# Optimization experiments

Measured on AMD Instinct MI355X. Metric: run time of the kernel, lower is better.

Reference implementation:

```python
import jax, jax.numpy as jnp
import numpy as np

H = 1024      # hidden_dim
NH = 8        # num_heads
DH = H // NH  # head dim = 128
IN = 512      # in_state_dim
CD = 256      # cond_dim
OUT = 512     # out_motion_dim
FH = 128      # FiLM hidden (hard-coded in _CondFiLM)
CLIP = 16.0   # input_clip
B, T = 2048, 32


def _ln(x, g, b, eps=1e-5):
    m = jnp.mean(x, axis=-1, keepdims=True)
    v = jnp.var(x, axis=-1, keepdims=True)
    return (x - m) * jax.lax.rsqrt(v + eps) * g + b


def setup_inputs() -> dict:
    key = jax.random.key(0)
    ks = jax.random.split(key, 16)
    w = lambda k, s: jax.random.normal(k, s, dtype=jnp.float32) * 0.02
    D = IN + CD
    return {
        'state': jax.random.normal(ks[0], (B, T, IN), dtype=jnp.float32),
        'cond': jax.random.normal(ks[1], (B, T, CD), dtype=jnp.float32),
        # shared_encoder: [Linear -> LayerNorm -> ReLU] x 2
        'ew1': w(ks[2], (D, H)), 'eb1': jnp.zeros((H,)), 'eg1': jnp.ones((H,)), 'ebt1': jnp.zeros((H,)),
        'ew2': w(ks[3], (H, H)), 'eb2': jnp.zeros((H,)), 'eg2': jnp.ones((H,)), 'ebt2': jnp.zeros((H,)),
        # residual_proj (input_dim != hidden_dim -> Linear)
        'rw': w(ks[4], (D, H)), 'rb': jnp.zeros((H,)),
        # FiLM conditioner
        'fw1': w(ks[5], (CD, FH)), 'fb1': jnp.zeros((FH,)),
        'fw2': w(ks[6], (FH, 2 * H)), 'fb2': jnp.zeros((2 * H,)),
        # query LayerNorm
        'lnq_g': jnp.ones((H,)), 'lnq_b': jnp.zeros((H,)),
        # attention projections (bias=False)
        'wq': w(ks[7], (H, H)), 'wk': w(ks[8], (H, H)), 'wv': w(ks[9], (H, H)), 'wo': w(ks[10], (H, H)),
        # coupling norm
        'cn_g': jnp.ones((H,)), 'cn_b': jnp.zeros((H,)),
        # motion head: Linear -> ReLU -> Linear
        'hw1': w(ks[11], (H, H)), 'hb1': jnp.zeros((H,)),
        'hw2': w(ks[12], (H, OUT)), 'hb2': jnp.zeros((OUT,)),
    }


def reference(state, cond, ew1, eb1, eg1, ebt1, ew2, eb2, eg2, ebt2, rw, rb,
              fw1, fb1, fw2, fb2, lnq_g, lnq_b, wq, wk, wv, wo, cn_g, cn_b,
              hw1, hb1, hw2, hb2):
    # input concat + guard clamp
    x = jnp.clip(jnp.concatenate([state, cond], axis=-1), -CLIP, CLIP)  # [B,T,D]
    # shared encoder
    h = jax.nn.relu(_ln(x @ ew1 + eb1, eg1, ebt1))
    h = jax.nn.relu(_ln(h @ ew2 + eb2, eg2, ebt2))                       # [B,T,H]
    res = x @ rw + rb                                                    # [B,T,H]
    # FiLM gain/bias from cond (exact-erf gelu to match torch F.gelu)
    fh = jax.nn.gelu(cond @ fw1 + fb1, approximate=False)
    g, b = jnp.split(fh @ fw2 + fb2, 2, axis=-1)
    g = 1.0 + 0.5 * jnp.tanh(g)
    b = 0.5 * jnp.tanh(b)
    # FiLM-gated query path
    qin = _ln(h, lnq_g, lnq_b) * g + b
    Bq, Tq, _ = h.shape
    q = (qin @ wq).reshape(Bq, Tq, NH, DH)
    k = (h @ wk).reshape(Bq, Tq, NH, DH)
    v = (h @ wv).reshape(Bq, Tq, NH, DH)
    scores = jnp.einsum('bqhd,bkhd->bhqk', q, k) / np.float32(np.sqrt(DH))
    attn = jax.nn.softmax(scores, axis=-1)
    o = jnp.einsum('bhqk,bkhd->bqhd', attn, v).reshape(Bq, Tq, H) @ wo
    # residual couple + norm
    h2 = _ln(h + o + res, cn_g, cn_b)
    # motion head
    m = jax.nn.relu(h2 @ hw1 + hb1)
    return m @ hw2 + hb2  # [B,T,out_motion_dim]
```

## Files before the change

### kernel.cpp

```cpp
#include <hip/hip_runtime.h>
#include <hip/hip_bf16.h>

typedef unsigned short u16;
typedef short bf16x8 __attribute__((ext_vector_type(8)));
typedef u16 u16x8 __attribute__((ext_vector_type(8)));
typedef float f32x4 __attribute__((ext_vector_type(4)));
typedef float f32x16 __attribute__((ext_vector_type(16)));

#define DEV __device__ __forceinline__

DEV u16 f2bf(float f) {
  union { float f; unsigned u; } a; a.f = f;
  unsigned r = a.u + 0x7FFFu + ((a.u >> 16) & 1u);
  return (u16)(r >> 16);
}
DEV float bf2f(u16 u) {
  union { unsigned u; float f; } a; a.u = ((unsigned)u) << 16; return a.f;
}
DEV float ftanh(float v) {
  float e = __expf(2.f * v);
  return 1.f - 2.f / (e + 1.f);
}
DEV void async16(const void* g, void* l) {
  __builtin_amdgcn_global_load_lds(
      (const __attribute__((address_space(1))) unsigned int*)g,
      (__attribute__((address_space(3))) unsigned int*)l, 16, 0, 0);
}

#define SBAR() asm volatile("s_barrier" ::: "memory")
#define WAITV(n) asm volatile("s_waitcnt vmcnt(" #n ")" ::: "memory")

__global__ __launch_bounds__(256) void transpose_cvt(const float* __restrict__ in,
                                                     u16* __restrict__ out, int K, int N) {
  __shared__ float tile[32][33];
  const int kt = blockIdx.y * 32, nt = blockIdx.x * 32;
  const int tx = threadIdx.x & 31, ty = threadIdx.x >> 5;
#pragma unroll
  for (int i = 0; i < 32; i += 8) {
    int k = kt + ty + i, n = nt + tx;
    tile[ty + i][tx] = (k < K && n < N) ? in[(long)k * N + n] : 0.f;
  }
  __syncthreads();
#pragma unroll
  for (int i = 0; i < 32; i += 8) {
    int n = nt + ty + i, k = kt + tx;
    if (n < N && k < K) out[(long)n * K + k] = f2bf(tile[tx][ty + i]);
  }
}

__global__ __launch_bounds__(256) void prep_kernel(const float* __restrict__ state,
                                                   const float* __restrict__ cond,
                                                   u16* __restrict__ xb) {
  int idx = blockIdx.x * 256 + threadIdx.x;
  int t = idx / 192, c4 = idx - t * 192;
  float4 v;
  if (c4 < 128) v = ((const float4*)state)[(long)t * 128 + c4];
  else          v = ((const float4*)cond)[(long)t * 64 + (c4 - 128)];
  ushort4 o;
  o.x = f2bf(fminf(fmaxf(v.x, -16.f), 16.f));
  o.y = f2bf(fminf(fmaxf(v.y, -16.f), 16.f));
  o.z = f2bf(fminf(fmaxf(v.z, -16.f), 16.f));
  o.w = f2bf(fminf(fmaxf(v.w, -16.f), 16.f));
  *(ushort4*)(xb + (long)t * 768 + c4 * 4) = o;
}

DEV void reduce2(float& s, float& q, float* sh, int tid) {
#pragma unroll
  for (int off = 32; off; off >>= 1) { s += __shfl_xor(s, off); q += __shfl_xor(q, off); }
  const int w = tid >> 6;
  if ((tid & 63) == 0) { sh[w] = s; sh[4 + w] = q; }
  __syncthreads();
  s = sh[0] + sh[1] + sh[2] + sh[3];
  q = sh[4] + sh[5] + sh[6] + sh[7];
}

__global__ __launch_bounds__(256) void ln_relu_kernel(const u16* in,
                                                      const float* __restrict__ g,
                                                      const float* __restrict__ bt,
                                                      u16* out) {
  __shared__ float sh[8];
  const long row = blockIdx.x;
  const int tid = threadIdx.x;
  ushort4 hv = *(const ushort4*)(in + row * 1024 + tid * 4);
  float x[4] = {bf2f(hv.x), bf2f(hv.y), bf2f(hv.z), bf2f(hv.w)};
  float s = x[0] + x[1] + x[2] + x[3];
  float q = x[0]*x[0] + x[1]*x[1] + x[2]*x[2] + x[3]*x[3];
  reduce2(s, q, sh, tid);
  float mean = s * (1.f / 1024.f);
  float var  = q * (1.f / 1024.f) - mean * mean;
  float rs   = rsqrtf(var + 1e-5f);
  ushort4 ov; u16* op = (u16*)&ov;
#pragma unroll
  for (int j = 0; j < 4; ++j) {
    int c = tid * 4 + j;
    float y = (x[j] - mean) * rs * g[c] + bt[c];
    op[j] = f2bf(fmaxf(y, 0.f));
  }
  *(ushort4*)(out + row * 1024 + tid * 4) = ov;
}

__global__ __launch_bounds__(256) void qin_gb_kernel(const u16* __restrict__ h,
                                                     const u16* gb,
                                                     const float* __restrict__ lg,
                                                     const float* __restrict__ lbt,
                                                     u16* qout) {
  __shared__ float sh[8];
  const long row = blockIdx.x;
  const int tid = threadIdx.x;
  ushort4 hv = *(const ushort4*)(h + row * 1024 + tid * 4);
  float x[4] = {bf2f(hv.x), bf2f(hv.y), bf2f(hv.z), bf2f(hv.w)};
  float s = x[0] + x[1] + x[2] + x[3];
  float q = x[0]*x[0] + x[1]*x[1] + x[2]*x[2] + x[3]*x[3];
  reduce2(s, q, sh, tid);
  float mean = s * (1.f / 1024.f);
  float var  = q * (1.f / 1024.f) - mean * mean;
  float rs   = rsqrtf(var + 1e-5f);
  ushort4 gv = *(const ushort4*)(gb + row * 2048 + tid * 4);
  ushort4 bv = *(const ushort4*)(gb + row * 2048 + 1024 + tid * 4);
  const u16* gp = (const u16*)&gv;
  const u16* bp = (const u16*)&bv;
  ushort4 ov; u16* op = (u16*)&ov;
#pragma unroll
  for (int j = 0; j < 4; ++j) {
    int c = tid * 4 + j;
    float y = (x[j] - mean) * rs * lg[c] + lbt[c];
    op[j] = f2bf(y * bf2f(gp[j]) + bf2f(bp[j]));
  }
  *(ushort4*)(qout + row * 1024 + tid * 4) = ov;
}

__global__ __launch_bounds__(256) void qin_sep_kernel(const u16* __restrict__ h,
                                                      const u16* gain, const u16* bias,
                                                      const float* __restrict__ lg,
                                                      const float* __restrict__ lbt,
                                                      u16* qout) {
  __shared__ float sh[8];
  const long row = blockIdx.x;
  const int tid = threadIdx.x;
  ushort4 hv = *(const ushort4*)(h + row * 1024 + tid * 4);
  float x[4] = {bf2f(hv.x), bf2f(hv.y), bf2f(hv.z), bf2f(hv.w)};
  float s = x[0] + x[1] + x[2] + x[3];
  float q = x[0]*x[0] + x[1]*x[1] + x[2]*x[2] + x[3]*x[3];
  reduce2(s, q, sh, tid);
  float mean = s * (1.f / 1024.f);
  float var  = q * (1.f / 1024.f) - mean * mean;
  float rs   = rsqrtf(var + 1e-5f);
  ushort4 gv = *(const ushort4*)(gain + row * 1024 + tid * 4);
  ushort4 bv = *(const ushort4*)(bias + row * 1024 + tid * 4);
  const u16* gp = (const u16*)&gv;
  const u16* bp = (const u16*)&bv;
  ushort4 ov; u16* op = (u16*)&ov;
#pragma unroll
  for (int j = 0; j < 4; ++j) {
    int c = tid * 4 + j;
    float y = (x[j] - mean) * rs * lg[c] + lbt[c];
    op[j] = f2bf(y * bf2f(gp[j]) + bf2f(bp[j]));
  }
  *(ushort4*)(qout + row * 1024 + tid * 4) = ov;
}

__global__ __launch_bounds__(256) void h2_kernel(const u16* __restrict__ h,
                                                 const u16* o2,
                                                 const float* __restrict__ g,
                                                 const float* __restrict__ bt,
                                                 u16* out) {
  __shared__ float sh[8];
  const long row = blockIdx.x;
  const int tid = threadIdx.x;
  ushort4 a = *(const ushort4*)(h  + row * 1024 + tid * 4);
  ushort4 b = *(const ushort4*)(o2 + row * 1024 + tid * 4);
  const u16* ap = (const u16*)&a; const u16* bp = (const u16*)&b;
  float x[4];
#pragma unroll
  for (int j = 0; j < 4; ++j) x[j] = bf2f(ap[j]) + bf2f(bp[j]);
  float s = x[0] + x[1] + x[2] + x[3];
  float q = x[0]*x[0] + x[1]*x[1] + x[2]*x[2] + x[3]*x[3];
  reduce2(s, q, sh, tid);
  float mean = s * (1.f / 1024.f);
  float var  = q * (1.f / 1024.f) - mean * mean;
  float rs   = rsqrtf(var + 1e-5f);
  ushort4 ov; u16* op = (u16*)&ov;
#pragma unroll
  for (int j = 0; j < 4; ++j) {
    int c = tid * 4 + j;
    op[j] = f2bf((x[j] - mean) * rs * g[c] + bt[c]);
  }
  *(ushort4*)(out + row * 1024 + tid * 4) = ov;
}

template <int EPI>
__global__ __launch_bounds__(256) void gemm_bt(const u16* __restrict__ A,
                                               const u16* __restrict__ Bt,
                                               const float* __restrict__ bias,
                                               const u16* addend,
                                               u16* Co, float* Cf,
                                               int N, int K, int lda) {
  __shared__ u16 As[128 * 64];
  __shared__ u16 Bs[128 * 64];
  const int tid = threadIdx.x;
  const int w = tid >> 6, l = tid & 63;
  const int wr = w >> 1, wc = w & 1;
  const long bRow = (long)blockIdx.x * 128;
  const long bCol = (long)blockIdx.y * 128;

  f32x4 acc[4][4];
#pragma unroll
  for (int mi = 0; mi < 4; ++mi)
#pragma unroll
    for (int ni = 0; ni < 4; ++ni) acc[mi][ni] = (f32x4){0.f, 0.f, 0.f, 0.f};

  const int arow = l >> 3;
  const int acol = (l & 7) * 8;
  const u16* gA = A + (bRow + w * 8 + arow) * (long)lda + acol;
  const u16* gB = Bt + (bCol + w * 8 + arow) * (long)K + acol;

  const int fr = l & 15;
  const int fks = (l >> 4) * 8;

  for (int kt = 0; kt < K; kt += 64) {
#pragma unroll
    for (int i = 0; i < 4; ++i) {
      async16(gA + (long)i * 32 * lda + kt, As + (i * 32 + w * 8) * 64);
      async16(gB + (long)i * 32 * K   + kt, Bs + (i * 32 + w * 8) * 64);
    }
    __syncthreads();
#pragma unroll
    for (int kk = 0; kk < 2; ++kk) {
      const int ko = kk * 32 + fks;
      bf16x8 af[4], bff[4];
#pragma unroll
      for (int mi = 0; mi < 4; ++mi)
        af[mi] = *(const bf16x8*)(As + (wr * 64 + mi * 16 + fr) * 64 + ko);
#pragma unroll
      for (int ni = 0; ni < 4; ++ni)
        bff[ni] = *(const bf16x8*)(Bs + (wc * 64 + ni * 16 + fr) * 64 + ko);
#pragma unroll
      for (int mi = 0; mi < 4; ++mi)
#pragma unroll
        for (int ni = 0; ni < 4; ++ni)
          acc[mi][ni] = __builtin_amdgcn_mfma_f32_16x16x32_bf16(af[mi], bff[ni], acc[mi][ni], 0, 0, 0);
    }
    __syncthreads();
  }

  const int fq = l >> 4;
#pragma unroll
  for (int ni = 0; ni < 4; ++ni) {
    const long col = bCol + wc * 64 + ni * 16 + fr;
    const float bs = bias ? bias[col] : 0.f;
#pragma unroll
    for (int mi = 0; mi < 4; ++mi) {
#pragma unroll
      for (int r = 0; r < 4; ++r) {
        const long row = bRow + wr * 64 + mi * 16 + fq * 4 + r;
        float v = acc[mi][ni][r] + bs;
        if (EPI == 1) v = 0.5f * v * (1.f + erff(v * 0.70710678118654752f));
        else if (EPI == 2) v = 1.f + 0.5f * ftanh(v);
        else if (EPI == 3) v = fmaxf(v, 0.f);
        else if (EPI == 5) v += bf2f(addend[row * N + col]);
        else if (EPI == 6) v = 0.5f * ftanh(v);
        if (EPI == 4) Cf[row * N + col] = v;
        else          Co[row * N + col] = f2bf(v);
      }
    }
  }
}


#define RDA(buf, Qr) do { \
  _Pragma("unroll") for (int ks_ = 0; ks_ < 2; ++ks_) \
  _Pragma("unroll") for (int m_ = 0; m_ < 4; ++m_) \
    a[ks_][m_] = *(const bf16x8*)(ldsc + (buf) * 32768 + \
      ((Qr) * 128 + wr * 64 + m_ * 16 + fr) * 128 + ((ks_ * 64 + fq * 16) ^ swzc)); \
} while (0)

#define RDB(buf, Qc) do { \
  _Pragma("unroll") for (int ks_ = 0; ks_ < 2; ++ks_) \
  _Pragma("unroll") for (int n_ = 0; n_ < 2; ++n_) \
    b[ks_][n_] = *(const bf16x8*)(ldsc + 65536 + (buf) * 32768 + \
      ((Qc) * 128 + wc * 32 + n_ * 16 + fr) * 128 + ((ks_ * 64 + fq * 16) ^ swzc)); \
} while (0)

#define MM(Qr, Qc) do { \
  __builtin_amdgcn_s_setprio(1); \
  _Pragma("unroll") for (int m_ = 0; m_ < 4; ++m_) \
  _Pragma("unroll") for (int n_ = 0; n_ < 2; ++n_) \
  _Pragma("unroll") for (int ks_ = 0; ks_ < 2; ++ks_) \
    acc[Qr][Qc][m_][n_] = __builtin_amdgcn_mfma_f32_16x16x32_bf16( \
        a[ks_][m_], b[ks_][n_], acc[Qr][Qc][m_][n_], 0, 0, 0); \
  __builtin_amdgcn_s_setprio(0); \
} while (0)

#define STA(buf, tt, h) do { \
  _Pragma("unroll") for (int j_ = 0; j_ < 2; ++j_) \
    async16(aB + ((long)j_ * 64 + (h) * 128) * lda_l + (tt) * 64, \
            ldsc + (buf) * 32768 + (h) * 16384 + (j_ * 512 + tid) * 16); \
} while (0)

#define STB(buf, tt, h) do { \
  _Pragma("unroll") for (int j_ = 0; j_ < 2; ++j_) \
    async16(bB + ((long)j_ * 64 + (h) * 128) * K_l + (tt) * 64, \
            ldsc + 65536 + (buf) * 32768 + (h) * 16384 + (j_ * 512 + tid) * 16); \
} while (0)

template <int EPI>
__global__ __launch_bounds__(512, 1) void gemm256(const u16* __restrict__ A,
                                                  const u16* __restrict__ Bt,
                                                  const float* __restrict__ bias,
                                                  const u16* addend,
                                                  u16* Co, u16* Co2, float* Cf,
                                                  int N, int K, int lda, int ctLog) {
  extern __shared__ char ldsc[];
  const int tid = threadIdx.x;
  const int l = tid & 63;
  const int w = tid >> 6, wr = w >> 2, wc = w & 3;
  const int fr = l & 15, fq = l >> 4;
  const int swzc = (fr & 7) << 4;
  const long lda_l = lda, K_l = K;

  const int nwg = gridDim.x;
  const int orig = blockIdx.x;
  const int swz = (orig & 7) * (nwg >> 3) + (orig >> 3);
  const int rt = swz >> ctLog, ct = swz & ((1 << ctLog) - 1);
  const long bRow = (long)rt * 256, bCol = (long)ct * 256;
  const int NT = K >> 6;

  const int L0 = tid * 16;
  const int row0 = L0 >> 7;
  const int cswz = (L0 & 127) ^ ((row0 & 7) << 4);
  const u16* aB = A + (bRow + row0) * lda_l + (cswz >> 1);
  const u16* bB = Bt + (bCol + row0) * K_l + (cswz >> 1);

  f32x4 acc[2][2][4][2];
#pragma unroll
  for (int p = 0; p < 2; ++p)
#pragma unroll
    for (int qq = 0; qq < 2; ++qq)
#pragma unroll
      for (int m = 0; m < 4; ++m)
#pragma unroll
        for (int n = 0; n < 2; ++n) acc[p][qq][m][n] = (f32x4){0.f, 0.f, 0.f, 0.f};

  bf16x8 a[2][4], b[2][2];

  STA(0, 0, 0); STA(0, 0, 1); STB(0, 0, 0); STB(0, 0, 1);
  STA(1, 1, 0); STB(1, 1, 1);
  WAITV(4);
  SBAR();

  for (int i = 0; i < (NT >> 1); ++i) {
    const int t0 = 2 * i, t1 = t0 + 1;
    const bool more = (t0 + 2) < NT;
    RDA(0, 0); RDB(0, 0);
    STA(1, t1, 1);
    SBAR(); MM(0, 0); SBAR();
    RDB(0, 1);
    STB(1, t1, 0);
    SBAR(); MM(0, 1); SBAR();
    RDA(0, 1);
    if (more) STA(0, t0 + 2, 0);
    SBAR(); MM(1, 1); SBAR();
    RDB(0, 0);
    if (more) STB(0, t0 + 2, 1);
    SBAR(); MM(1, 0);
    if (more) { WAITV(4); } else { WAITV(0); }
    SBAR();
    RDA(1, 0); RDB(1, 0);
    if (more) STA(0, t0 + 2, 1);
    SBAR(); MM(0, 0); SBAR();
    RDB(1, 1);
    if (more) STB(0, t0 + 2, 0);
    SBAR(); MM(0, 1); SBAR();
    RDA(1, 1);
    if (more) STA(1, t1 + 2, 0);
    SBAR(); MM(1, 1); SBAR();
    RDB(1, 0);
    if (more) STB(1, t1 + 2, 1);
    SBAR(); MM(1, 0);
    if (more) { WAITV(4); } else { WAITV(0); }
    SBAR();
  }

  if (EPI != 4) {
    u16* dst = Co; long colBase = bCol; long strideW = N;
    if (EPI == 6) {
      strideW = 1024;
      if (bCol >= 1024) { dst = Co2; colBase = bCol - 1024; }
    }
    const bool gainHalf = (bCol < 1024);
    u16* lds16 = (u16*)ldsc;
#pragma unroll
    for (int Qr = 0; Qr < 2; ++Qr)
#pragma unroll
      for (int Qc = 0; Qc < 2; ++Qc)
#pragma unroll
        for (int n = 0; n < 2; ++n) {
          const int colL = Qc * 128 + wc * 32 + n * 16 + fr;
          const float bs = bias ? bias[bCol + colL] : 0.f;
#pragma unroll
          for (int m = 0; m < 4; ++m)
#pragma unroll
            for (int r = 0; r < 4; ++r) {
              const int rowL = Qr * 128 + wr * 64 + m * 16 + fq * 4 + r;
              float v = acc[Qr][Qc][m][n][r] + bs;
              if (EPI == 2)      { float t = ftanh(v); v = gainHalf ? 1.f + 0.5f * t : 0.5f * t; }
              else if (EPI == 3) v = fmaxf(v, 0.f);
              lds16[rowL * 256 + colL] = f2bf(v);
            }
        }
    __syncthreads();
    const int rB = tid >> 5, cL = (tid & 31) * 8;
#pragma unroll
    for (int it = 0; it < 16; ++it) {
      const int rL = it * 16 + rB;
      const long gr = bRow + rL;
      u16x8 sv = *(const u16x8*)(lds16 + rL * 256 + cL);
      if (EPI == 5) {
        u16x8 ad = *(const u16x8*)(addend + gr * (long)N + bCol + cL);
#pragma unroll
        for (int j = 0; j < 8; ++j) sv[j] = f2bf(bf2f(sv[j]) + bf2f(ad[j]));
      }
      *(u16x8*)(dst + gr * strideW + colBase + cL) = sv;
    }
  } else {
    float* ldsf = (float*)ldsc;
#pragma unroll
    for (int p = 0; p < 2; ++p) {
#pragma unroll
      for (int Qc = 0; Qc < 2; ++Qc)
#pragma unroll
        for (int n = 0; n < 2; ++n) {
          const int colL = Qc * 128 + wc * 32 + n * 16 + fr;
          const float bs = bias ? bias[bCol + colL] : 0.f;
#pragma unroll
          for (int m = 0; m < 4; ++m)
#pragma unroll
            for (int r = 0; r < 4; ++r) {
              const int rowL = wr * 64 + m * 16 + fq * 4 + r;
              ldsf[rowL * 256 + colL] = acc[p][Qc][m][n][r] + bs;
            }
        }
      __syncthreads();
      const int c4 = (tid & 63) * 4, rB = tid >> 6;
#pragma unroll
      for (int it = 0; it < 16; ++it) {
        const int rL = it * 8 + rB;
        const long gr = bRow + p * 128 + rL;
        float4 fv = *(const float4*)(ldsf + rL * 256 + c4);
        *(float4*)(Cf + gr * (long)N + bCol + c4) = fv;
      }
      __syncthreads();
    }
  }
}

__global__ __launch_bounds__(64) void attn_kernel(const u16* q,
                                                  const u16* __restrict__ k,
                                                  const u16* __restrict__ v,
                                                  u16* o) {
  const int bh = blockIdx.x;
  const int b = bh >> 3, hd = bh & 7;
  const long base = (long)b * 32 * 1024 + hd * 128;
  const int l = threadIdx.x, lo = l & 31, hi = l >> 5;
  __shared__ u16 P[32 * 36];
  __shared__ u16 Vt[128 * 36];

#pragma unroll
  for (int i = 0; i < 8; ++i) {
    int idx = i * 64 + l;
    int tok = idx >> 4, d0 = (idx & 15) * 8;
    const u16* src = v + base + (long)tok * 1024 + d0;
    ushort4 a0 = *(const ushort4*)src;
    ushort4 a1 = *(const ushort4*)(src + 4);
    u16 vals[8] = {a0.x, a0.y, a0.z, a0.w, a1.x, a1.y, a1.z, a1.w};
#pragma unroll
    for (int j = 0; j < 8; ++j) Vt[(d0 + j) * 36 + tok] = vals[j];
  }

  f32x16 st;
#pragma unroll
  for (int r = 0; r < 16; ++r) st[r] = 0.f;
#pragma unroll
  for (int kb = 0; kb < 8; ++kb) {
    bf16x8 kf = *(const bf16x8*)(k + base + (long)lo * 1024 + kb * 16 + hi * 8);
    bf16x8 qf = *(const bf16x8*)(q + base + (long)lo * 1024 + kb * 16 + hi * 8);
    st = __builtin_amdgcn_mfma_f32_32x32x16_bf16(kf, qf, st, 0, 0, 0);
  }
  float mx = -1e30f;
#pragma unroll
  for (int r = 0; r < 16; ++r) { st[r] *= 0.08838834764831845f; mx = fmaxf(mx, st[r]); }
  mx = fmaxf(mx, __shfl_xor(mx, 32));
  float p[16], sum = 0.f;
#pragma unroll
  for (int r = 0; r < 16; ++r) { p[r] = __expf(st[r] - mx); sum += p[r]; }
  sum += __shfl_xor(sum, 32);
  const float inv = 1.f / sum;
#pragma unroll
  for (int r = 0; r < 16; ++r) {
    int kt = (r & 3) + 8 * (r >> 2) + 4 * hi;
    P[lo * 36 + kt] = f2bf(p[r] * inv);
  }
  __syncthreads();

#pragma unroll
  for (int nb = 0; nb < 4; ++nb) {
    f32x16 oa;
#pragma unroll
    for (int r = 0; r < 16; ++r) oa[r] = 0.f;
#pragma unroll
    for (int ks = 0; ks < 2; ++ks) {
      union { bf16x8 v8; ushort4 h[2]; } pa, vb;
      pa.h[0] = *(const ushort4*)&P[lo * 36 + ks * 16 + hi * 8];
      pa.h[1] = *(const ushort4*)&P[lo * 36 + ks * 16 + hi * 8 + 4];
      vb.h[0] = *(const ushort4*)&Vt[(nb * 32 + lo) * 36 + ks * 16 + hi * 8];
      vb.h[1] = *(const ushort4*)&Vt[(nb * 32 + lo) * 36 + ks * 16 + hi * 8 + 4];
      oa = __builtin_amdgcn_mfma_f32_32x32x16_bf16(pa.v8, vb.v8, oa, 0, 0, 0);
    }
#pragma unroll
    for (int r = 0; r < 16; ++r) {
      int qrow = (r & 3) + 8 * (r >> 2) + 4 * hi;
      o[base + (long)qrow * 1024 + nb * 32 + lo] = f2bf(oa[r]);
    }
  }
}

extern "C" void kernel_launch(void* const* d_in, const int* in_sizes, int n_in,
                              void* d_out, int out_size, void* d_ws, size_t ws_size,
                              hipStream_t stream) {
  const float* state = (const float*)d_in[0];  const float* cond  = (const float*)d_in[1];
  const float* ew1 = (const float*)d_in[2];    const float* eb1 = (const float*)d_in[3];
  const float* eg1 = (const float*)d_in[4];    const float* ebt1 = (const float*)d_in[5];
  const float* ew2 = (const float*)d_in[6];    const float* eb2 = (const float*)d_in[7];
  const float* eg2 = (const float*)d_in[8];    const float* ebt2 = (const float*)d_in[9];
  const float* rw = (const float*)d_in[10];    const float* rb = (const float*)d_in[11];
  const float* fw1 = (const float*)d_in[12];   const float* fb1 = (const float*)d_in[13];
  const float* fw2 = (const float*)d_in[14];   const float* fb2 = (const float*)d_in[15];
  const float* lnq_g = (const float*)d_in[16]; const float* lnq_b = (const float*)d_in[17];
  const float* wq = (const float*)d_in[18];    const float* wk = (const float*)d_in[19];
  const float* wv = (const float*)d_in[20];    const float* wo = (const float*)d_in[21];
  const float* cn_g = (const float*)d_in[22];  const float* cn_b = (const float*)d_in[23];
  const float* hw1 = (const float*)d_in[24];   const float* hb1 = (const float*)d_in[25];
  const float* hw2 = (const float*)d_in[26];   const float* hb2 = (const float*)d_in[27];

  const size_t MB128 = 134217728ULL;
  const size_t WT_BYTES = 17367040ULL;
  const size_t FH_BYTES = 16777216ULL;
  char* ws = (char*)d_ws;
  u16* OUTu = (u16*)d_out;
  float* OUTf = (float*)d_out;

  (void)hipFuncSetAttribute((const void*)gemm256<0>, hipFuncAttributeMaxDynamicSharedMemorySize, 131072);
  (void)hipFuncSetAttribute((const void*)gemm256<2>, hipFuncAttributeMaxDynamicSharedMemorySize, 131072);
  (void)hipFuncSetAttribute((const void*)gemm256<3>, hipFuncAttributeMaxDynamicSharedMemorySize, 131072);
  (void)hipFuncSetAttribute((const void*)gemm256<4>, hipFuncAttributeMaxDynamicSharedMemorySize, 131072);
  (void)hipFuncSetAttribute((const void*)gemm256<5>, hipFuncAttributeMaxDynamicSharedMemorySize, 131072);
  (void)hipFuncSetAttribute((const void*)gemm256<6>, hipFuncAttributeMaxDynamicSharedMemorySize, 131072);

  u16* wt = nullptr;
  bool planA = false;
  int R = 0;
  if (ws_size >= 3 * MB128 + FH_BYTES + WT_BYTES) {
    planA = true;
    wt = (u16*)(ws + 3 * MB128 + FH_BYTES);
  } else {
    for (int r = 8192; r >= 1024; r >>= 1) {
      size_t need = 2 * MB128 + (size_t)r * 8448ULL + WT_BYTES;
      if (ws_size >= need) { R = r; wt = (u16*)(ws + 2 * MB128 + (size_t)r * 8448ULL); break; }
    }
    if (!R) return;
  }

  u16* ew1T = wt + 0;        u16* rwT  = wt + 786432;  u16* ew2T = wt + 1572864;
  u16* fw1T = wt + 2621440;  u16* fw2T = wt + 2654208;
  u16* wqT  = wt + 2916352;  u16* wkT  = wt + 3964928; u16* wvT  = wt + 5013504;
  u16* woT  = wt + 6062080;  u16* hw1T = wt + 7110656; u16* hw2T = wt + 8159232;

  transpose_cvt<<<dim3(32, 24), 256, 0, stream>>>(ew1, ew1T, 768, 1024);
  transpose_cvt<<<dim3(32, 24), 256, 0, stream>>>(rw,  rwT,  768, 1024);
  transpose_cvt<<<dim3(32, 32), 256, 0, stream>>>(ew2, ew2T, 1024, 1024);
  transpose_cvt<<<dim3(4, 8),   256, 0, stream>>>(fw1, fw1T, 256, 128);
  transpose_cvt<<<dim3(64, 4),  256, 0, stream>>>(fw2, fw2T, 128, 2048);
  transpose_cvt<<<dim3(32, 32), 256, 0, stream>>>(wq, wqT, 1024, 1024);
  transpose_cvt<<<dim3(32, 32), 256, 0, stream>>>(wk, wkT, 1024, 1024);
  transpose_cvt<<<dim3(32, 32), 256, 0, stream>>>(wv, wvT, 1024, 1024);
  transpose_cvt<<<dim3(32, 32), 256, 0, stream>>>(wo, woT, 1024, 1024);
  transpose_cvt<<<dim3(32, 32), 256, 0, stream>>>(hw1, hw1T, 1024, 1024);
  transpose_cvt<<<dim3(16, 32), 256, 0, stream>>>(hw2, hw2T, 1024, 512);

  if (planA) {
    u16* S1 = (u16*)ws;
    u16* S2 = (u16*)(ws + MB128);
    u16* S3 = (u16*)(ws + 2 * MB128);
    u16* FH = (u16*)(ws + 3 * MB128);

    prep_kernel<<<49152, 256, 0, stream>>>(state, cond, S1);
    gemm_bt<1><<<dim3(512, 1), 256, 0, stream>>>(S1 + 512, fw1T, fb1, nullptr, FH, nullptr, 128, 256, 768);
    gemm256<0><<<1024, 512, 131072, stream>>>(S1, ew1T, eb1, nullptr, S2, nullptr, nullptr, 1024, 768, 768, 2);
    ln_relu_kernel<<<65536, 256, 0, stream>>>(S2, eg1, ebt1, S2);
    gemm256<0><<<1024, 512, 131072, stream>>>(S2, ew2T, eb2, nullptr, S3, nullptr, nullptr, 1024, 1024, 1024, 2);
    ln_relu_kernel<<<65536, 256, 0, stream>>>(S3, eg2, ebt2, S3);
    gemm256<2><<<2048, 512, 131072, stream>>>(FH, fw2T, fb2, nullptr, S1, nullptr, nullptr, 2048, 128, 128, 3);
    qin_gb_kernel<<<65536, 256, 0, stream>>>(S3, S1, lnq_g, lnq_b, OUTu);
    gemm256<0><<<1024, 512, 131072, stream>>>(OUTu, wqT, nullptr, nullptr, S1, nullptr, nullptr, 1024, 1024, 1024, 2);
    gemm256<6><<<2048, 512, 131072, stream>>>(S3, wkT, nullptr, nullptr, S2, OUTu, nullptr, 2048, 1024, 1024, 3);
    attn_kernel<<<16384, 64, 0, stream>>>(S1, S2, OUTu, S1);
    prep_kernel<<<49152, 256, 0, stream>>>(state, cond, S2);
    gemm256<0><<<1024, 512, 131072, stream>>>(S2, rwT, rb, nullptr, OUTu, nullptr, nullptr, 1024, 768, 768, 2);
    gemm256<5><<<1024, 512, 131072, stream>>>(S1, woT, nullptr, OUTu, OUTu, nullptr, nullptr, 1024, 1024, 1024, 2);
    h2_kernel<<<65536, 256, 0, stream>>>(S3, OUTu, cn_g, cn_b, S1);
    gemm256<3><<<1024, 512, 131072, stream>>>(S1, hw1T, hb1, nullptr, S2, nullptr, nullptr, 1024, 1024, 1024, 2);
    gemm256<4><<<512, 512, 131072, stream>>>(S2, hw2T, hb2, nullptr, nullptr, nullptr, OUTf, 512, 1024, 1024, 1);
    return;
  }

  u16* F1 = (u16*)ws;
  u16* F2 = (u16*)(ws + MB128);
  char* g = ws + 2 * MB128;
  u16* G0 = (u16*)g;
  u16* G1 = (u16*)(g + (size_t)R * 2048);
  u16* G2 = (u16*)(g + (size_t)R * 4096);
  u16* G3 = (u16*)(g + (size_t)R * 4096 + (size_t)R * 256);
  u16* G4 = (u16*)(g + (size_t)R * 6144 + (size_t)R * 256);
  const int GX = R / 128, CH = 65536 / R;

  for (int c = 0; c < CH; ++c) {
    const long r0 = (long)c * R;
    prep_kernel<<<R * 3 / 4, 256, 0, stream>>>(state + r0 * 512, cond + r0 * 256, G0);
    gemm_bt<1><<<dim3(GX, 1), 256, 0, stream>>>(G0 + 512, fw1T, fb1, nullptr, G2, nullptr, 128, 256, 768);
    gemm_bt<0><<<dim3(GX, 8), 256, 0, stream>>>(G0, ew1T, eb1, nullptr, G1, nullptr, 1024, 768, 768);
    gemm_bt<0><<<dim3(GX, 8), 256, 0, stream>>>(G0, rwT,  rb,  nullptr, F2 + r0 * 1024, nullptr, 1024, 768, 768);
    ln_relu_kernel<<<R, 256, 0, stream>>>(G1, eg1, ebt1, G3);
    gemm_bt<0><<<dim3(GX, 8), 256, 0, stream>>>(G3, ew2T, eb2, nullptr, G0, nullptr, 1024, 1024, 1024);
    ln_relu_kernel<<<R, 256, 0, stream>>>(G0, eg2, ebt2, F1 + r0 * 1024);
    gemm_bt<2><<<dim3(GX, 8), 256, 0, stream>>>(G2, fw2T, fb2, nullptr, G3, nullptr, 1024, 128, 128);
    gemm_bt<6><<<dim3(GX, 8), 256, 0, stream>>>(G2, fw2T + 131072, fb2 + 1024, nullptr, G1, nullptr, 1024, 128, 128);
    qin_sep_kernel<<<R, 256, 0, stream>>>(F1 + r0 * 1024, G3, G1, lnq_g, lnq_b, G3);
    gemm_bt<0><<<dim3(GX, 8), 256, 0, stream>>>(G3, wqT, nullptr, nullptr, G0, nullptr, 1024, 1024, 1024);
    gemm_bt<0><<<dim3(GX, 8), 256, 0, stream>>>(F1 + r0 * 1024, wkT, nullptr, nullptr, G1, nullptr, 1024, 1024, 1024);
    gemm_bt<0><<<dim3(GX, 8), 256, 0, stream>>>(F1 + r0 * 1024, wvT, nullptr, nullptr, G4, nullptr, 1024, 1024, 1024);
    attn_kernel<<<(R / 32) * 8, 64, 0, stream>>>(G0, G1, G4, G0);
    gemm_bt<5><<<dim3(GX, 8), 256, 0, stream>>>(G0, woT, nullptr, F2 + r0 * 1024, F2 + r0 * 1024, nullptr, 1024, 1024, 1024);
  }
  h2_kernel<<<65536, 256, 0, stream>>>(F1, F2, cn_g, cn_b, OUTu);
  gemm_bt<3><<<dim3(512, 8), 256, 0, stream>>>(OUTu, hw1T, hb1, nullptr, F1, nullptr, 1024, 1024, 1024);
  gemm_bt<4><<<dim3(512, 4), 256, 0, stream>>>(F1, hw2T, hb2, nullptr, nullptr, OUTf, 512, 1024, 1024);
}
```

Measured before the change: 2.090 ms.

## Fuse FiLM second projection into query LayerNorm and use wave-per-row LayerNorm kernels

The FiLM fw2 GEMM (with its tanh epilogue) is folded into a new film_qin kernel. It loads 32 rows of h into LDS, computes per-row LN statistics, runs MFMA on the 128-wide FiLM hidden against fw2T, and applies the gain and bias directly. This avoids writing and rereading the 2048-wide gain/bias tensor. The LayerNorm+ReLU and h2 kernels are rewritten to process one row per wavefront with 16 elements per lane, which removes the block-level shared-memory reduction and barrier. Risks: film_qin uses about 74KB of LDS and only 2048 blocks, and it rereads fw2T from global memory for every block.

Result: faster. 2.000 ms (-4.3%).

```diff
diff --git a/kernel.cpp b/kernel.cpp
--- a/kernel.cpp
+++ b/kernel.cpp
@@ -64,69 +64,85 @@
   *(ushort4*)(xb + (long)t * 768 + c4 * 4) = o;
 }
 
-DEV void reduce2(float& s, float& q, float* sh, int tid) {
+DEV void wreduce2(float& s, float& q) {
 #pragma unroll
   for (int off = 32; off; off >>= 1) { s += __shfl_xor(s, off); q += __shfl_xor(q, off); }
-  const int w = tid >> 6;
-  if ((tid & 63) == 0) { sh[w] = s; sh[4 + w] = q; }
-  __syncthreads();
-  s = sh[0] + sh[1] + sh[2] + sh[3];
-  q = sh[4] + sh[5] + sh[6] + sh[7];
-}
-
-__global__ __launch_bounds__(256) void ln_relu_kernel(const u16* in,
-                                                      const float* __restrict__ g,
-                                                      const float* __restrict__ bt,
-                                                      u16* out) {
-  __shared__ float sh[8];
-  const long row = blockIdx.x;
-  const int tid = threadIdx.x;
-  ushort4 hv = *(const ushort4*)(in + row * 1024 + tid * 4);
-  float x[4] = {bf2f(hv.x), bf2f(hv.y), bf2f(hv.z), bf2f(hv.w)};
-  float s = x[0] + x[1] + x[2] + x[3];
-  float q = x[0]*x[0] + x[1]*x[1] + x[2]*x[2] + x[3]*x[3];
-  reduce2(s, q, sh, tid);
+}
+
+__global__ __launch_bounds__(256) void ln_relu_w(const u16* in,
+                                                 const float* __restrict__ g,
+                                                 const float* __restrict__ bt,
+                                                 u16* out) {
+  const int wid = threadIdx.x >> 6, lane = threadIdx.x & 63;
+  const long row = (long)blockIdx.x * 4 + wid;
+  const u16* ip = in + row * 1024 + lane * 16;
+  u16x8 v0 = *(const u16x8*)ip;
+  u16x8 v1 = *(const u16x8*)(ip + 8);
+  float x[16];
+#pragma unroll
+  for (int j = 0; j < 8; ++j) { x[j] = bf2f(v0[j]); x[8 + j] = bf2f(v1[j]); }
+  float s = 0.f, q = 0.f;
+#pragma unroll
+  for (int j = 0; j < 16; ++j) { s += x[j]; q += x[j] * x[j]; }
+  wreduce2(s, q);
   float mean = s * (1.f / 1024.f);
   float var  = q * (1.f / 1024.f) - mean * mean;
   float rs   = rsqrtf(var + 1e-5f);
-  ushort4 ov; u16* op = (u16*)&ov;
-#pragma unroll
-  for (int j = 0; j < 4; ++j) {
-    int c = tid * 4 + j;
-    float y = (x[j] - mean) * rs * g[c] + bt[c];
-    op[j] = f2bf(fmaxf(y, 0.f));
-  }
-  *(ushort4*)(out + row * 1024 + tid * 4) = ov;
-}
-
-__global__ __launch_bounds__(256) void qin_gb_kernel(const u16* __restrict__ h,
-                                                     const u16* gb,
-                                                     const float* __restrict__ lg,
-                                                     const float* __restrict__ lbt,
-                                                     u16* qout) {
-  __shared__ float sh[8];
-  const long row = blockIdx.x;
-  const int tid = threadIdx.x;
-  ushort4 hv = *(const ushort4*)(h + row * 1024 + tid * 4);
-  float x[4] = {bf2f(hv.x), bf2f(hv.y), bf2f(hv.z), bf2f(hv.w)};
-  float s = x[0] + x[1] + x[2] + x[3];
-  float q = x[0]*x[0] + x[1]*x[1] + x[2]*x[2] + x[3]*x[3];
-  reduce2(s, q, sh, tid);
+  const int c0 = lane * 16;
+  float4 g0 = *(const float4*)(g + c0),      g1 = *(const float4*)(g + c0 + 4);
+  float4 g2 = *(const float4*)(g + c0 + 8),  g3 = *(const float4*)(g + c0 + 12);
+  float4 b0 = *(const float4*)(bt + c0),     b1 = *(const float4*)(bt + c0 + 4);
+  float4 b2 = *(const float4*)(bt + c0 + 8), b3 = *(const float4*)(bt + c0 + 12);
+  const float* gp = (const float*)&g0; (void)g1; (void)g2; (void)g3;
+  const float* bp = (const float*)&b0; (void)b1; (void)b2; (void)b3;
+  float ga[16] = {g0.x,g0.y,g0.z,g0.w, g1.x,g1.y,g1.z,g1.w, g2.x,g2.y,g2.z,g2.w, g3.x,g3.y,g3.z,g3.w};
+  float ba[16] = {b0.x,b0.y,b0.z,b0.w, b1.x,b1.y,b1.z,b1.w, b2.x,b2.y,b2.z,b2.w, b3.x,b3.y,b3.z,b3.w};
+  (void)gp; (void)bp;
+  u16x8 o0, o1;
+#pragma unroll
+  for (int j = 0; j < 8; ++j) {
+    o0[j] = f2bf(fmaxf((x[j] - mean) * rs * ga[j] + ba[j], 0.f));
+    o1[j] = f2bf(fmaxf((x[8 + j] - mean) * rs * ga[8 + j] + ba[8 + j], 0.f));
+  }
+  u16* op = out + row * 1024 + lane * 16;
+  *(u16x8*)op = o0;
+  *(u16x8*)(op + 8) = o1;
+}
+
+__global__ __launch_bounds__(256) void h2_w(const u16* __restrict__ h,
+                                            const u16* o2,
+                                            const float* __restrict__ g,
+                                            const float* __restrict__ bt,
+                                            u16* out) {
+  const int wid = threadIdx.x >> 6, lane = threadIdx.x & 63;
+  const long row = (long)blockIdx.x * 4 + wid;
+  const u16* hp = h + row * 1024 + lane * 16;
+  const u16* op2 = o2 + row * 1024 + lane * 16;
+  u16x8 a0 = *(const u16x8*)hp,  a1 = *(const u16x8*)(hp + 8);
+  u16x8 c0v = *(const u16x8*)op2, c1v = *(const u16x8*)(op2 + 8);
+  float x[16];
+#pragma unroll
+  for (int j = 0; j < 8; ++j) {
+    x[j]     = bf2f(a0[j]) + bf2f(c0v[j]);
+    x[8 + j] = bf2f(a1[j]) + bf2f(c1v[j]);
+  }
+  float s = 0.f, q = 0.f;
+#pragma unroll
+  for (int j = 0; j < 16; ++j) { s += x[j]; q += x[j] * x[j]; }
+  wreduce2(s, q);
   float mean = s * (1.f / 1024.f);
   float var  = q * (1.f / 1024.f) - mean * mean;
   float rs   = rsqrtf(var + 1e-5f);
-  ushort4 gv = *(const ushort4*)(gb + row * 2048 + tid * 4);
-  ushort4 bv = *(const ushort4*)(gb + row * 2048 + 1024 + tid * 4);
-  const u16* gp = (const u16*)&gv;
-  const u16* bp = (const u16*)&bv;
-  ushort4 ov; u16* op = (u16*)&ov;
-#pragma unroll
-  for (int j = 0; j < 4; ++j) {
-    int c = tid * 4 + j;
-    float y = (x[j] - mean) * rs * lg[c] + lbt[c];
-    op[j] = f2bf(y * bf2f(gp[j]) + bf2f(bp[j]));
-  }
-  *(ushort4*)(qout + row * 1024 + tid * 4) = ov;
+  const int cc = lane * 16;
+  u16x8 o0, o1;
+#pragma unroll
+  for (int j = 0; j < 8; ++j) {
+    o0[j] = f2bf((x[j] - mean) * rs * g[cc + j] + bt[cc + j]);
+    o1[j] = f2bf((x[8 + j] - mean) * rs * g[cc + 8 + j] + bt[cc + 8 + j]);
+  }
+  u16* op = out + row * 1024 + lane * 16;
+  *(u16x8*)op = o0;
+  *(u16x8*)(op + 8) = o1;
 }
 
 __global__ __launch_bounds__(256) void qin_sep_kernel(const u16* __restrict__ h,
@@ -141,7 +157,13 @@
   float x[4] = {bf2f(hv.x), bf2f(hv.y), bf2f(hv.z), bf2f(hv.w)};
   float s = x[0] + x[1] + x[2] + x[3];
   float q = x[0]*x[0] + x[1]*x[1] + x[2]*x[2] + x[3]*x[3];
-  reduce2(s, q, sh, tid);
+#pragma unroll
+  for (int off = 32; off; off >>= 1) { s += __shfl_xor(s, off); q += __shfl_xor(q, off); }
+  const int w = tid >> 6;
+  if ((tid & 63) == 0) { sh[w] = s; sh[4 + w] = q; }
+  __syncthreads();
+  s = sh[0] + sh[1] + sh[2] + sh[3];
+  q = sh[4] + sh[5] + sh[6] + sh[7];
   float mean = s * (1.f / 1024.f);
   float var  = q * (1.f / 1024.f) - mean * mean;
   float rs   = rsqrtf(var + 1e-5f);
@@ -159,33 +181,98 @@
   *(ushort4*)(qout + row * 1024 + tid * 4) = ov;
 }
 
-__global__ __launch_bounds__(256) void h2_kernel(const u16* __restrict__ h,
-                                                 const u16* o2,
-                                                 const float* __restrict__ g,
-                                                 const float* __restrict__ bt,
-                                                 u16* out) {
-  __shared__ float sh[8];
-  const long row = blockIdx.x;
+__global__ __launch_bounds__(256) void film_qin(const u16* __restrict__ hbf,
+                                                const u16* __restrict__ fh,
+                                                const u16* __restrict__ fw2T,
+                                                const float* __restrict__ fb2,
+                                                const float* __restrict__ lg,
+                                                const float* __restrict__ lbt,
+                                                u16* __restrict__ qout) {
+  extern __shared__ char lds[];
+  u16* H = (u16*)lds;
+  char* Afh = lds + 65536;
+  float* sLN = (float*)(lds + 73728);
   const int tid = threadIdx.x;
-  ushort4 a = *(const ushort4*)(h  + row * 1024 + tid * 4);
-  ushort4 b = *(const ushort4*)(o2 + row * 1024 + tid * 4);
-  const u16* ap = (const u16*)&a; const u16* bp = (const u16*)&b;
-  float x[4];
-#pragma unroll
-  for (int j = 0; j < 4; ++j) x[j] = bf2f(ap[j]) + bf2f(bp[j]);
-  float s = x[0] + x[1] + x[2] + x[3];
-  float q = x[0]*x[0] + x[1]*x[1] + x[2]*x[2] + x[3]*x[3];
-  reduce2(s, q, sh, tid);
-  float mean = s * (1.f / 1024.f);
-  float var  = q * (1.f / 1024.f) - mean * mean;
-  float rs   = rsqrtf(var + 1e-5f);
-  ushort4 ov; u16* op = (u16*)&ov;
-#pragma unroll
-  for (int j = 0; j < 4; ++j) {
-    int c = tid * 4 + j;
-    op[j] = f2bf((x[j] - mean) * rs * g[c] + bt[c]);
-  }
-  *(ushort4*)(out + row * 1024 + tid * 4) = ov;
+  const int wid = tid >> 6, lane = tid & 63;
+  const int fr = lane & 15, fq = lane >> 4;
+  const long rows0 = (long)blockIdx.x * 32;
+
+  {
+    const int row = tid >> 3;
+    const int inner = (tid & 7) * 32;
+    const u16* src = fh + (rows0 + row) * 128 + (tid & 7) * 16;
+    u16x8 f0 = *(const u16x8*)src;
+    u16x8 f1 = *(const u16x8*)(src + 8);
+    *(u16x8*)(Afh + row * 256 + ((inner)      ^ ((row & 7) << 4))) = f0;
+    *(u16x8*)(Afh + row * 256 + ((inner + 16) ^ ((row & 7) << 4))) = f1;
+  }
+
+#pragma unroll
+  for (int i = 0; i < 8; ++i) {
+    const int row = i * 4 + wid;
+    const u16* src = hbf + (rows0 + row) * 1024 + lane * 16;
+    u16x8 v0 = *(const u16x8*)src;
+    u16x8 v1 = *(const u16x8*)(src + 8);
+    *(u16x8*)(H + row * 1024 + lane * 16) = v0;
+    *(u16x8*)(H + row * 1024 + lane * 16 + 8) = v1;
+    float s = 0.f, q = 0.f;
+#pragma unroll
+    for (int j = 0; j < 8; ++j) {
+      float x0 = bf2f(v0[j]), x1 = bf2f(v1[j]);
+      s += x0 + x1; q += x0 * x0 + x1 * x1;
+    }
+    wreduce2(s, q);
+    if (lane == 0) {
+      float mean = s * (1.f / 1024.f);
+      float var  = q * (1.f / 1024.f) - mean * mean;
+      sLN[row * 2] = mean;
+      sLN[row * 2 + 1] = rsqrtf(var + 1e-5f);
+    }
+  }
+  __syncthreads();
+
+  const int cbase = wid * 256;
+#pragma unroll 1
+  for (int c8 = 0; c8 < 16; ++c8) {
+    const int c = cbase + c8 * 16;
+    const int col = c + fr;
+    f32x4 ag[2] = {{0.f,0.f,0.f,0.f},{0.f,0.f,0.f,0.f}};
+    f32x4 ab[2] = {{0.f,0.f,0.f,0.f},{0.f,0.f,0.f,0.f}};
+#pragma unroll
+    for (int ks = 0; ks < 4; ++ks) {
+      bf16x8 bg = *(const bf16x8*)(fw2T + (long)col * 128 + ks * 32 + fq * 8);
+      bf16x8 bb = *(const bf16x8*)(fw2T + (long)(1024 + col) * 128 + ks * 32 + fq * 8);
+#pragma unroll
+      for (int t = 0; t < 2; ++t) {
+        const int row = t * 16 + fr;
+        bf16x8 av = *(const bf16x8*)(Afh + row * 256 + ((ks * 64 + fq * 16) ^ ((fr & 7) << 4)));
+        ag[t] = __builtin_amdgcn_mfma_f32_16x16x32_bf16(av, bg, ag[t], 0, 0, 0);
+        ab[t] = __builtin_amdgcn_mfma_f32_16x16x32_bf16(av, bb, ab[t], 0, 0, 0);
+      }
+    }
+    const float fg = fb2[col], fb = fb2[1024 + col];
+    const float lgc = lg[col], lbc = lbt[col];
+#pragma unroll
+    for (int t = 0; t < 2; ++t)
+#pragma unroll
+      for (int r = 0; r < 4; ++r) {
+        const int row = t * 16 + fq * 4 + r;
+        float gv = 1.f + 0.5f * ftanh(ag[t][r] + fg);
+        float bv = 0.5f * ftanh(ab[t][r] + fb);
+        float x = bf2f(H[row * 1024 + col]);
+        float y = (x - sLN[row * 2]) * sLN[row * 2 + 1] * lgc + lbc;
+        H[row * 1024 + col] = f2bf(y * gv + bv);
+      }
+  }
+  __syncthreads();
+
+#pragma unroll
+  for (int i = 0; i < 8; ++i) {
+    const int row = i * 4 + wid;
+    u16* dst = qout + (rows0 + row) * 1024 + lane * 16;
+    *(u16x8*)dst = *(const u16x8*)(H + row * 1024 + lane * 16);
+    *(u16x8*)(dst + 8) = *(const u16x8*)(H + row * 1024 + lane * 16 + 8);
+  }
 }
 
 template <int EPI>
@@ -265,7 +352,6 @@
     }
   }
 }
-
 
 #define RDA(buf, Qr) do { \
   _Pragma("unroll") for (int ks_ = 0; ks_ < 2; ++ks_) \
@@ -387,7 +473,6 @@
       strideW = 1024;
       if (bCol >= 1024) { dst = Co2; colBase = bCol - 1024; }
     }
-    const bool gainHalf = (bCol < 1024);
     u16* lds16 = (u16*)ldsc;
 #pragma unroll
     for (int Qr = 0; Qr < 2; ++Qr)
@@ -403,8 +488,7 @@
             for (int r = 0; r < 4; ++r) {
               const int rowL = Qr * 128 + wr * 64 + m * 16 + fq * 4 + r;
               float v = acc[Qr][Qc][m][n][r] + bs;
-              if (EPI == 2)      { float t = ftanh(v); v = gainHalf ? 1.f + 0.5f * t : 0.5f * t; }
-              else if (EPI == 3) v = fmaxf(v, 0.f);
+              if (EPI == 3) v = fmaxf(v, 0.f);
               lds16[rowL * 256 + colL] = f2bf(v);
             }
         }
@@ -550,11 +634,11 @@
   float* OUTf = (float*)d_out;
 
   (void)hipFuncSetAttribute((const void*)gemm256<0>, hipFuncAttributeMaxDynamicSharedMemorySize, 131072);
-  (void)hipFuncSetAttribute((const void*)gemm256<2>, hipFuncAttributeMaxDynamicSharedMemorySize, 131072);
   (void)hipFuncSetAttribute((const void*)gemm256<3>, hipFuncAttributeMaxDynamicSharedMemorySize, 131072);
   (void)hipFuncSetAttribute((const void*)gemm256<4>, hipFuncAttributeMaxDynamicSharedMemorySize, 131072);
   (void)hipFuncSetAttribute((const void*)gemm256<5>, hipFuncAttributeMaxDynamicSharedMemorySize, 131072);
   (void)hipFuncSetAttribute((const void*)gemm256<6>, hipFuncAttributeMaxDynamicSharedMemorySize, 131072);
+  (void)hipFuncSetAttribute((const void*)film_qin,   hipFuncAttributeMaxDynamicSharedMemorySize, 73984);
 
   u16* wt = nullptr;
   bool planA = false;
@@ -596,18 +680,17 @@
     prep_kernel<<<49152, 256, 0, stream>>>(state, cond, S1);
     gemm_bt<1><<<dim3(512, 1), 256, 0, stream>>>(S1 + 512, fw1T, fb1, nullptr, FH, nullptr, 128, 256, 768);
     gemm256<0><<<1024, 512, 131072, stream>>>(S1, ew1T, eb1, nullptr, S2, nullptr, nullptr, 1024, 768, 768, 2);
-    ln_relu_kernel<<<65536, 256, 0, stream>>>(S2, eg1, ebt1, S2);
+    ln_relu_w<<<16384, 256, 0, stream>>>(S2, eg1, ebt1, S2);
     gemm256<0><<<1024, 512, 131072, stream>>>(S2, ew2T, eb2, nullptr, S3, nullptr, nullptr, 1024, 1024, 1024, 2);
-    ln_relu_kernel<<<65536, 256, 0, stream>>>(S3, eg2, ebt2, S3);
-    gemm256<2><<<2048, 512, 131072, stream>>>(FH, fw2T, fb2, nullptr, S1, nullptr, nullptr, 2048, 128, 128, 3);
-    qin_gb_kernel<<<65536, 256, 0, stream>>>(S3, S1, lnq_g, lnq_b, OUTu);
+    ln_relu_w<<<16384, 256, 0, stream>>>(S3, eg2, ebt2, S3);
+    film_qin<<<2048, 256, 73984, stream>>>(S3, FH, fw2T, fb2, lnq_g, lnq_b, OUTu);
     gemm256<0><<<1024, 512, 131072, stream>>>(OUTu, wqT, nullptr, nullptr, S1, nullptr, nullptr, 1024, 1024, 1024, 2);
     gemm256<6><<<2048, 512, 131072, stream>>>(S3, wkT, nullptr, nullptr, S2, OUTu, nullptr, 2048, 1024, 1024, 3);
     attn_kernel<<<16384, 64, 0, stream>>>(S1, S2, OUTu, S1);
     prep_kernel<<<49152, 256, 0, stream>>>(state, cond, S2);
     gemm256<0><<<1024, 512, 131072, stream>>>(S2, rwT, rb, nullptr, OUTu, nullptr, nullptr, 1024, 768, 768, 2);
     gemm256<5><<<1024, 512, 131072, stream>>>(S1, woT, nullptr, OUTu, OUTu, nullptr, nullptr, 1024, 1024, 1024, 2);
-    h2_kernel<<<65536, 256, 0, stream>>>(S3, OUTu, cn_g, cn_b, S1);
+    h2_w<<<16384, 256, 0, stream>>>(S3, OUTu, cn_g, cn_b, S1);
     gemm256<3><<<1024, 512, 131072, stream>>>(S1, hw1T, hb1, nullptr, S2, nullptr, nullptr, 1024, 1024, 1024, 2);
     gemm256<4><<<512, 512, 131072, stream>>>(S2, hw2T, hb2, nullptr, nullptr, nullptr, OUTf, 512, 1024, 1024, 1);
     return;
@@ -629,9 +712,9 @@
     gemm_bt<1><<<dim3(GX, 1), 256, 0, stream>>>(G0 + 512, fw1T, fb1, nullptr, G2, nullptr, 128, 256, 768);
     gemm_bt<0><<<dim3(GX, 8), 256, 0, stream>>>(G0, ew1T, eb1, nullptr, G1, nullptr, 1024, 768, 768);
     gemm_bt<0><<<dim3(GX, 8), 256, 0, stream>>>(G0, rwT,  rb,  nullptr, F2 + r0 * 1024, nullptr, 1024, 768, 768);
-    ln_relu_kernel<<<R, 256, 0, stream>>>(G1, eg1, ebt1, G3);
+    ln_relu_w<<<R / 4, 256, 0, stream>>>(G1, eg1, ebt1, G3);
     gemm_bt<0><<<dim3(GX, 8), 256, 0, stream>>>(G3, ew2T, eb2, nullptr, G0, nullptr, 1024, 1024, 1024);
-    ln_relu_kernel<<<R, 256, 0, stream>>>(G0, eg2, ebt2, F1 + r0 * 1024);
+    ln_relu_w<<<R / 4, 256, 0, stream>>>(G0, eg2, ebt2, F1 + r0 * 1024);
     gemm_bt<2><<<dim3(GX, 8), 256, 0, stream>>>(G2, fw2T, fb2, nullptr, G3, nullptr, 1024, 128, 128);
     gemm_bt<6><<<dim3(GX, 8), 256, 0, stream>>>(G2, fw2T + 131072, fb2 + 1024, nullptr, G1, nullptr, 1024, 128, 128);
     qin_sep_kernel<<<R, 256, 0, stream>>>(F1 + r0 * 1024, G3, G1, lnq_g, lnq_b, G3);
@@ -641,7 +724,7 @@
     attn_kernel<<<(R / 32) * 8, 64, 0, stream>>>(G0, G1, G4, G0);
     gemm_bt<5><<<dim3(GX, 8), 256, 0, stream>>>(G0, woT, nullptr, F2 + r0 * 1024, F2 + r0 * 1024, nullptr, 1024, 1024, 1024);
   }
-  h2_kernel<<<65536, 256, 0, stream>>>(F1, F2, cn_g, cn_b, OUTu);
+  h2_w<<<16384, 256, 0, stream>>>(F1, F2, cn_g, cn_b, OUTu);
   gemm_bt<3><<<dim3(512, 8), 256, 0, stream>>>(OUTu, hw1T, hb1, nullptr, F1, nullptr, 1024, 1024, 1024);
   gemm_bt<4><<<dim3(512, 4), 256, 0, stream>>>(F1, hw2T, hb2, nullptr, nullptr, OUTf, 512, 1024, 1024);
 }
```
